# Kernel optimization log

Measured on AMD Instinct MI355X. Metric: run time of the kernel, lower is better.

## Reference

```python
import jax, jax.numpy as jnp
import numpy as np

L = 2            # decoder layers (layer slice)
H = 1024         # hidden size
NH = 16          # attention heads
HD = 64          # head dim
NKV = 4          # kv heads (GQA)
KVD = NKV * HD   # 256
I = 2816         # intermediate size
V = 32000        # vocab
R = 64           # lora rank
S = 512          # seq len
B = 1            # batch
BLK = 64         # quantization block size
NCODE = 16       # 2**k codebook entries (k=4)
LORA_S = 16.0 / 64.0  # lora_alpha / lora_r
EPS = 1e-6
THETA = 10000.0


def _dequant(idx2d, am, codebook):
    # blockwise k-bit dequant: w[i] = codebook[idx[i]] * absmax[i // BLK]
    n, k = idx2d.shape
    w = codebook[idx2d.reshape(-1)].reshape(-1, BLK) * am[:, None]
    return w.reshape(n, k)


def _linear(x, idx, am, codebook, A, Bm):
    # fused dequant-matmul + low-rank LoRA update
    w = _dequant(idx, am, codebook)           # [N, K]
    return x @ w.T + LORA_S * ((x @ A.T) @ Bm.T)


def _rmsnorm(x, w):
    return x * jax.lax.rsqrt(jnp.mean(x * x, axis=-1, keepdims=True) + EPS) * w


def _rope_cache():
    inv_freq = 1.0 / (THETA ** (np.arange(0, HD, 2, dtype=np.float32) / HD))
    freqs = np.outer(np.arange(S, dtype=np.float32), inv_freq)
    emb = np.concatenate([freqs, freqs], axis=-1)  # [S, HD]
    return jnp.asarray(np.cos(emb)), jnp.asarray(np.sin(emb))


def _apply_rope(x, cos, sin):
    # x: [B, S, n_heads, HD]; llama-style non-interleaved rotate_half
    x1, x2 = jnp.split(x, 2, axis=-1)
    rot = jnp.concatenate([-x2, x1], axis=-1)
    return x * cos[None, :, None, :] + rot * sin[None, :, None, :]


def _forward(input_ids, embed, codebook, q_idx, q_am, qA, qB, k_idx, k_am, kA, kB,
             v_idx, v_am, vA, vB, o_idx, o_am, oA, oB, g_idx, g_am, gA, gB,
             u_idx, u_am, uA, uB, d_idx, d_am, dA, dB, ln1, ln2, final_norm,
             lm_idx, lm_am):
    cos, sin = _rope_cache()
    mask = jnp.tril(jnp.ones((S, S), dtype=bool))
    h = embed[input_ids]  # [B, S, H]
    for i in range(L):
        # --- attention block ---
        x = _rmsnorm(h, ln1[i])
        q = _linear(x, q_idx[i], q_am[i], codebook, qA[i], qB[i]).reshape(B, S, NH, HD)
        k = _linear(x, k_idx[i], k_am[i], codebook, kA[i], kB[i]).reshape(B, S, NKV, HD)
        v = _linear(x, v_idx[i], v_am[i], codebook, vA[i], vB[i]).reshape(B, S, NKV, HD)
        q = _apply_rope(q, cos, sin)
        k = _apply_rope(k, cos, sin)
        k = jnp.repeat(k, NH // NKV, axis=2)  # GQA expand
        v = jnp.repeat(v, NH // NKV, axis=2)
        scores = jnp.einsum('bqhd,bkhd->bhqk', q, k) / np.float32(np.sqrt(HD))
        scores = jnp.where(mask[None, None], scores, jnp.float32(-1e30))
        attn = jax.nn.softmax(scores, axis=-1)
        ctx = jnp.einsum('bhqk,bkhd->bqhd', attn, v).reshape(B, S, H)
        h = h + _linear(ctx, o_idx[i], o_am[i], codebook, oA[i], oB[i])
        # --- SwiGLU MLP block ---
        x = _rmsnorm(h, ln2[i])
        gate = _linear(x, g_idx[i], g_am[i], codebook, gA[i], gB[i])
        up = _linear(x, u_idx[i], u_am[i], codebook, uA[i], uB[i])
        h = h + _linear(jax.nn.silu(gate) * up, d_idx[i], d_am[i], codebook, dA[i], dB[i])
    h = _rmsnorm(h, final_norm)
    logits = h @ _dequant(lm_idx, lm_am, codebook).T  # quantized lm_head, no LoRA
    return logits


def setup_inputs():
    key = jax.random.key(0)
    keys = iter(jax.random.split(key, 80))
    def idx(shape):
        return jax.random.randint(next(keys), shape, 0, NCODE, dtype=jnp.int32)
    def amL(nblocks):
        return jax.random.uniform(next(keys), (L, nblocks), dtype=jnp.float32) * 0.02 + 1e-3
    def lora(shape):
        return jax.random.normal(next(keys), shape, dtype=jnp.float32) * 0.02
    inp = {}
    inp['input_ids'] = jax.random.randint(next(keys), (B, S), 0, V, dtype=jnp.int32)
    inp['embed'] = jax.random.normal(next(keys), (V, H), dtype=jnp.float32) * 0.02
    inp['codebook'] = jnp.linspace(-1.0, 1.0, NCODE, dtype=jnp.float32)
    inp['q_idx'] = idx((L, H, H));    inp['q_am'] = amL(H * H // BLK)
    inp['qA'] = lora((L, R, H));      inp['qB'] = lora((L, H, R))
    inp['k_idx'] = idx((L, KVD, H));  inp['k_am'] = amL(KVD * H // BLK)
    inp['kA'] = lora((L, R, H));      inp['kB'] = lora((L, KVD, R))
    inp['v_idx'] = idx((L, KVD, H));  inp['v_am'] = amL(KVD * H // BLK)
    inp['vA'] = lora((L, R, H));      inp['vB'] = lora((L, KVD, R))
    inp['o_idx'] = idx((L, H, H));    inp['o_am'] = amL(H * H // BLK)
    inp['oA'] = lora((L, R, H));      inp['oB'] = lora((L, H, R))
    inp['g_idx'] = idx((L, I, H));    inp['g_am'] = amL(I * H // BLK)
    inp['gA'] = lora((L, R, H));      inp['gB'] = lora((L, I, R))
    inp['u_idx'] = idx((L, I, H));    inp['u_am'] = amL(I * H // BLK)
    inp['uA'] = lora((L, R, H));      inp['uB'] = lora((L, I, R))
    inp['d_idx'] = idx((L, H, I));    inp['d_am'] = amL(H * I // BLK)
    inp['dA'] = lora((L, R, I));      inp['dB'] = lora((L, H, R))
    inp['ln1'] = jnp.ones((L, H), dtype=jnp.float32)
    inp['ln2'] = jnp.ones((L, H), dtype=jnp.float32)
    inp['final_norm'] = jnp.ones((H,), dtype=jnp.float32)
    inp['lm_idx'] = idx((V, H))
    inp['lm_am'] = jax.random.uniform(next(keys), (V * H // BLK,), dtype=jnp.float32) * 0.02 + 1e-3
    return inp


def reference(input_ids, embed, codebook, q_idx, q_am, qA, qB, k_idx, k_am, kA, kB,
              v_idx, v_am, vA, vB, o_idx, o_am, oA, oB, g_idx, g_am, gA, gB,
              u_idx, u_am, uA, uB, d_idx, d_am, dA, dB, ln1, ln2, final_norm,
              lm_idx, lm_am):
    return _forward(input_ids, embed, codebook, q_idx, q_am, qA, qB, k_idx, k_am, kA, kB,
                    v_idx, v_am, vA, vB, o_idx, o_am, oA, oB, g_idx, g_am, gA, gB,
                    u_idx, u_am, uA, uB, d_idx, d_am, dA, dB, ln1, ln2, final_norm,
                    lm_idx, lm_am)
```

## Files before the change

kernel.cpp:

```cpp
#include <hip/hip_runtime.h>
#include <math.h>

constexpr int LAYERS = 2;
constexpr int H      = 1024;
constexpr int NH     = 16;
constexpr int HD     = 64;
constexpr int NKV    = 4;
constexpr int KVD    = 256;
constexpr int IDIM   = 2816;
constexpr int VOCAB  = 32000;
constexpr int RR     = 64;
constexpr int SEQ    = 512;
constexpr float LORA_SCALE = 0.25f;
constexpr float RMS_EPS    = 1e-6f;

typedef __attribute__((ext_vector_type(8))) __bf16 bf16x8;
typedef __attribute__((ext_vector_type(4))) __bf16 bf16x4;
typedef __attribute__((ext_vector_type(4))) float f32x4;

__device__ __forceinline__ float dot4(float4 a, float4 b) {
    return a.x*b.x + a.y*b.y + a.z*b.z + a.w*b.w;
}

__device__ __forceinline__ bf16x8 pack8(float4 a, float4 b) {
    bf16x8 p;
    p[0] = (__bf16)a.x; p[1] = (__bf16)a.y; p[2] = (__bf16)a.z; p[3] = (__bf16)a.w;
    p[4] = (__bf16)b.x; p[5] = (__bf16)b.y; p[6] = (__bf16)b.z; p[7] = (__bf16)b.w;
    return p;
}

__device__ __forceinline__ bf16x8 dq8(int4 a, int4 b, float amv, const float* cbs) {
    bf16x8 p;
    p[0] = (__bf16)(cbs[a.x]*amv); p[1] = (__bf16)(cbs[a.y]*amv);
    p[2] = (__bf16)(cbs[a.z]*amv); p[3] = (__bf16)(cbs[a.w]*amv);
    p[4] = (__bf16)(cbs[b.x]*amv); p[5] = (__bf16)(cbs[b.y]*amv);
    p[6] = (__bf16)(cbs[b.z]*amv); p[7] = (__bf16)(cbs[b.w]*amv);
    return p;
}

__global__ __launch_bounds__(256) void k_embed(const int* __restrict__ ids,
                                               const float* __restrict__ embed,
                                               float* __restrict__ h) {
    int s = blockIdx.x;
    int t = threadIdx.x;
    const float4* src = (const float4*)(embed + (size_t)ids[s] * H);
    float4* dst = (float4*)(h + (size_t)s * H);
    dst[t] = src[t];
}

__global__ __launch_bounds__(256) void k_rmsnorm(const float* __restrict__ h,
                                                 const float* __restrict__ w,
                                                 __bf16* __restrict__ x) {
    __shared__ float red[4];
    int s = blockIdx.x, t = threadIdx.x;
    float4 a = ((const float4*)(h + (size_t)s * H))[t];
    float ss = a.x*a.x + a.y*a.y + a.z*a.z + a.w*a.w;
    #pragma unroll
    for (int o = 32; o > 0; o >>= 1) ss += __shfl_xor(ss, o, 64);
    if ((t & 63) == 0) red[t >> 6] = ss;
    __syncthreads();
    float tot = red[0] + red[1] + red[2] + red[3];
    float scale = rsqrtf(tot * (1.0f / H) + RMS_EPS);
    float4 wv = ((const float4*)w)[t];
    bf16x4 o4;
    o4[0] = (__bf16)(a.x*scale*wv.x); o4[1] = (__bf16)(a.y*scale*wv.y);
    o4[2] = (__bf16)(a.z*scale*wv.z); o4[3] = (__bf16)(a.w*scale*wv.w);
    *(bf16x4*)&x[(size_t)s * H + t * 4] = o4;
}

struct GSeg {
    const int* widx; const float* am; const float* lA; const float* lB;
    float* y; int N; int ntiles;
};

template<int NSEG, bool LORA, int EPI, int KSPLIT>
__global__ __launch_bounds__(256) void k_gemm(
    const __bf16* __restrict__ x, const float* __restrict__ cb,
    GSeg s0, GSeg s1, GSeg s2, int K, int ntTotal, __bf16* __restrict__ y2)
{
    __shared__ __align__(16) __bf16 As[128][64];
    __shared__ __align__(16) __bf16 Bs[128][64];
    __shared__ __align__(16) __bf16 La[LORA ? 64 : 1][64];
    __shared__ float cbs[16];

    const int id = blockIdx.x + (blockIdx.y << 2);
    const int mtile = (id >> 3) & 3;
    int n = ((id >> 5) << 3) + (id & 7);
    if (n >= ntTotal) return;

    const int* widx; const float* am; const float* lA; const float* lB;
    float* y; int N;
    if (NSEG == 1 || n < s0.ntiles) {
        widx=s0.widx; am=s0.am; lA=s0.lA; lB=s0.lB; y=s0.y; N=s0.N;
    } else if (NSEG == 2 || (n - s0.ntiles) < s1.ntiles) {
        n -= s0.ntiles;
        widx=s1.widx; am=s1.am; lA=s1.lA; lB=s1.lB; y=s1.y; N=s1.N;
    } else {
        n -= s0.ntiles + s1.ntiles;
        widx=s2.widx; am=s2.am; lA=s2.lA; lB=s2.lB; y=s2.y; N=s2.N;
    }
    const int sbase = mtile * 128;
    const int nbase = n * 128;
    const int t    = threadIdx.x;
    const int lane = t & 63;
    const int wave = t >> 6;
    const int wm = (wave >> 1) * 64;
    const int wn = (wave & 1) * 64;
    if (t < 16) cbs[t] = cb[t];
    const int srow = t >> 3;
    const int scol = (t & 7) * 8;
    const int KB   = K >> 6;

    int kbLo, kbHi;
    if constexpr (KSPLIT > 1) {
        kbLo = ((int)blockIdx.z * KB) / KSPLIT;
        kbHi = (((int)blockIdx.z + 1) * KB) / KSPLIT;
    } else { kbLo = 0; kbHi = KB; }

    f32x4 acc[4][4];
    f32x4 accl[4][4];
    const f32x4 fz = {0.f, 0.f, 0.f, 0.f};
    #pragma unroll
    for (int i = 0; i < 4; ++i)
        #pragma unroll
        for (int j = 0; j < 4; ++j) { acc[i][j] = fz; if constexpr (LORA) accl[i][j] = fz; }

    __syncthreads();

    for (int kb = kbLo; kb < kbHi; ++kb) {
        const int k0 = kb << 6;
        #pragma unroll
        for (int p = 0; p < 4; ++p) {
            int row = p * 32 + srow;
            *(bf16x8*)&As[row][scol] =
                *(const bf16x8*)&x[(size_t)(sbase + row) * K + k0 + scol];
        }
        #pragma unroll
        for (int p = 0; p < 4; ++p) {
            int row = p * 32 + srow;
            const int* ip = &widx[(size_t)(nbase + row) * K + k0 + scol];
            int4 i0 = *(const int4*)ip;
            int4 i1 = *(const int4*)(ip + 4);
            float amv = am[(size_t)(nbase + row) * KB + kb];
            *(bf16x8*)&Bs[row][scol] = dq8(i0, i1, amv, cbs);
        }
        if constexpr (LORA) {
            #pragma unroll
            for (int p = 0; p < 2; ++p) {
                int r = p * 32 + srow;
                const float* lp = &lA[(size_t)r * K + k0 + scol];
                *(bf16x8*)&La[r][scol] = pack8(*(const float4*)lp, *(const float4*)(lp + 4));
            }
        }
        __syncthreads();
        #pragma unroll
        for (int s = 0; s < 2; ++s) {
            bf16x8 a[4], b[4];
            #pragma unroll
            for (int mi = 0; mi < 4; ++mi)
                a[mi] = *(bf16x8*)&As[wm + mi*16 + (lane & 15)][s*32 + (lane >> 4)*8];
            #pragma unroll
            for (int ni = 0; ni < 4; ++ni)
                b[ni] = *(bf16x8*)&Bs[wn + ni*16 + (lane & 15)][s*32 + (lane >> 4)*8];
            #pragma unroll
            for (int mi = 0; mi < 4; ++mi)
                #pragma unroll
                for (int ni = 0; ni < 4; ++ni)
                    acc[mi][ni] = __builtin_amdgcn_mfma_f32_16x16x32_bf16(
                        a[mi], b[ni], acc[mi][ni], 0, 0, 0);
            if constexpr (LORA) {
                bf16x8 bl[4];
                #pragma unroll
                for (int ni = 0; ni < 4; ++ni)
                    bl[ni] = *(bf16x8*)&La[ni*16 + (lane & 15)][s*32 + (lane >> 4)*8];
                #pragma unroll
                for (int mi = 0; mi < 4; ++mi)
                    #pragma unroll
                    for (int ni = 0; ni < 4; ++ni)
                        accl[mi][ni] = __builtin_amdgcn_mfma_f32_16x16x32_bf16(
                            a[mi], bl[ni], accl[mi][ni], 0, 0, 0);
            }
        }
        __syncthreads();
    }

    if constexpr (LORA) {
        if (wn == 0) {
            const int cr = (lane >> 4) * 4, cc = lane & 15;
            #pragma unroll
            for (int mi = 0; mi < 4; ++mi)
                #pragma unroll
                for (int ni = 0; ni < 4; ++ni)
                    #pragma unroll
                    for (int r = 0; r < 4; ++r)
                        As[wm + mi*16 + cr + r][ni*16 + cc] =
                            (__bf16)(LORA_SCALE * accl[mi][ni][r]);
        }
        #pragma unroll
        for (int p = 0; p < 4; ++p) {
            int row = p * 32 + srow;
            const float* bp = &lB[(size_t)(nbase + row) * RR + scol];
            *(bf16x8*)&Bs[row][scol] = pack8(*(const float4*)bp, *(const float4*)(bp + 4));
        }
        __syncthreads();
        #pragma unroll
        for (int s = 0; s < 2; ++s) {
            bf16x8 a[4], b[4];
            #pragma unroll
            for (int mi = 0; mi < 4; ++mi)
                a[mi] = *(bf16x8*)&As[wm + mi*16 + (lane & 15)][s*32 + (lane >> 4)*8];
            #pragma unroll
            for (int ni = 0; ni < 4; ++ni)
                b[ni] = *(bf16x8*)&Bs[wn + ni*16 + (lane & 15)][s*32 + (lane >> 4)*8];
            #pragma unroll
            for (int mi = 0; mi < 4; ++mi)
                #pragma unroll
                for (int ni = 0; ni < 4; ++ni)
                    acc[mi][ni] = __builtin_amdgcn_mfma_f32_16x16x32_bf16(
                        a[mi], b[ni], acc[mi][ni], 0, 0, 0);
        }
    }

    const int cr = (lane >> 4) * 4;
    const int cc = lane & 15;
    #pragma unroll
    for (int mi = 0; mi < 4; ++mi) {
        #pragma unroll
        for (int ni = 0; ni < 4; ++ni) {
            int gr = sbase + wm + mi * 16 + cr;
            int gc = nbase + wn + ni * 16 + cc;
            #pragma unroll
            for (int r = 0; r < 4; ++r) {
                size_t off = (size_t)(gr + r) * N + gc;
                if constexpr (EPI == 0) {
                    if constexpr (KSPLIT > 1) atomicAdd(&y[off], acc[mi][ni][r]);
                    else                      y[off] = acc[mi][ni][r];
                }
                if constexpr (EPI == 1) {
                    if constexpr (KSPLIT > 1) atomicAdd(&y[off], acc[mi][ni][r]);
                    else                      y[off] += acc[mi][ni][r];
                }
            }
        }
    }
    (void)y2;
}

__global__ __launch_bounds__(256) void k_silu(const float* __restrict__ g,
                                              const float* __restrict__ u,
                                              __bf16* __restrict__ out, int n4) {
    int i = blockIdx.x * 256 + threadIdx.x;
    int stride = gridDim.x * 256;
    for (; i < n4; i += stride) {
        float4 gv = ((const float4*)g)[i];
        float4 uv = ((const float4*)u)[i];
        bf16x4 o4;
        o4[0] = (__bf16)(gv.x / (1.f + __expf(-gv.x)) * uv.x);
        o4[1] = (__bf16)(gv.y / (1.f + __expf(-gv.y)) * uv.y);
        o4[2] = (__bf16)(gv.z / (1.f + __expf(-gv.z)) * uv.z);
        o4[3] = (__bf16)(gv.w / (1.f + __expf(-gv.w)) * uv.w);
        *(bf16x4*)&out[(size_t)i * 4] = o4;
    }
}

__global__ __launch_bounds__(256) void k_rope(float* __restrict__ q, float* __restrict__ k) {
    int s  = blockIdx.x;
    int hs = blockIdx.y * 4 + (threadIdx.x >> 6);
    int d  = threadIdx.x & 63;
    float* p = (hs < NH) ? q + ((size_t)s * NH + hs) * HD
                         : k + ((size_t)s * NKV + (hs - NH)) * HD;
    int j = d & 31;
    float inv = exp2f(-(float)(2 * j) * (13.287712379549449f / 64.0f));
    float ang = (float)s * inv;
    float sn, c;
    __sincosf(ang, &sn, &c);
    float xv = p[d];
    float other = (d < 32) ? -p[d + 32] : p[d - 32];
    p[d] = xv * c + other * sn;
}

__global__ __launch_bounds__(256) void k_scores(const float* __restrict__ q,
                                                const float* __restrict__ k,
                                                float* __restrict__ attn) {
    int qt = blockIdx.x;
    int h  = blockIdx.y;
    int kvh = h >> 2;
    __shared__ float qs[16][68];
    __shared__ float ks[64][68];
    __shared__ float sc[16][528];
    int t = threadIdx.x;
    { int row = t >> 4; int c4 = (t & 15) << 2;
      *(float4*)&qs[row][c4] = *(const float4*)&q[(size_t)(qt*16 + row) * H + h * HD + c4]; }
    for (int c = 0; c < 8; ++c) {
        #pragma unroll
        for (int i = 0; i < 4; ++i) {
            int id = t + i * 256; int row = id >> 4; int c4 = (id & 15) << 2;
            *(float4*)&ks[row][c4] = *(const float4*)&k[(size_t)(c*64 + row) * KVD + kvh * HD + c4];
        }
        __syncthreads();
        int r  = t >> 4;
        int cc = (t & 15) << 2;
        float4 acc = make_float4(0.f, 0.f, 0.f, 0.f);
        #pragma unroll
        for (int kk = 0; kk < 64; kk += 4) {
            float4 a = *(const float4*)&qs[r][kk];
            acc.x += dot4(a, *(const float4*)&ks[cc + 0][kk]);
            acc.y += dot4(a, *(const float4*)&ks[cc + 1][kk]);
            acc.z += dot4(a, *(const float4*)&ks[cc + 2][kk]);
            acc.w += dot4(a, *(const float4*)&ks[cc + 3][kk]);
        }
        acc.x *= 0.125f; acc.y *= 0.125f; acc.z *= 0.125f; acc.w *= 0.125f;
        *(float4*)&sc[r][c * 64 + cc] = acc;
        __syncthreads();
    }
    int r = t >> 4, lane = t & 15;
    int qpos = qt * 16 + r;
    float mx = -1e30f;
    for (int c = lane; c < SEQ; c += 16) if (c <= qpos) mx = fmaxf(mx, sc[r][c]);
    #pragma unroll
    for (int o = 8; o > 0; o >>= 1) mx = fmaxf(mx, __shfl_xor(mx, o, 16));
    float sum = 0.f;
    for (int c = lane; c < SEQ; c += 16) {
        float e = (c <= qpos) ? __expf(sc[r][c] - mx) : 0.f;
        sc[r][c] = e; sum += e;
    }
    #pragma unroll
    for (int o = 8; o > 0; o >>= 1) sum += __shfl_xor(sum, o, 16);
    float inv = 1.0f / sum;
    for (int c = lane; c < SEQ; c += 16)
        attn[((size_t)h * SEQ + qpos) * SEQ + c] = sc[r][c] * inv;
}

__global__ __launch_bounds__(256) void k_ctx(const float* __restrict__ attn,
                                             const float* __restrict__ v,
                                             __bf16* __restrict__ ctx) {
    int qt = blockIdx.x, h = blockIdx.y, kvh = h >> 2;
    __shared__ float as_[64][68];
    __shared__ float vs[64][68];
    int t = threadIdx.x;
    float acc[4][4] = {};
    for (int c = 0; c <= qt; ++c) {
        #pragma unroll
        for (int i = 0; i < 4; ++i) {
            int id = t + i * 256; int row = id >> 4; int c4 = (id & 15) << 2;
            *(float4*)&as_[row][c4] = *(const float4*)&attn[((size_t)h*SEQ + qt*64 + row) * SEQ + c*64 + c4];
            *(float4*)&vs[row][c4]  = *(const float4*)&v[(size_t)(c*64 + row) * KVD + kvh * HD + c4];
        }
        __syncthreads();
        int ty = (t >> 4) * 4, tx = (t & 15) * 4;
        #pragma unroll
        for (int kk = 0; kk < 64; ++kk) {
            float4 b = *(const float4*)&vs[kk][tx];
            #pragma unroll
            for (int i = 0; i < 4; ++i) {
                float a = as_[ty + i][kk];
                acc[i][0] += a * b.x; acc[i][1] += a * b.y;
                acc[i][2] += a * b.z; acc[i][3] += a * b.w;
            }
        }
        __syncthreads();
    }
    int ty = (t >> 4) * 4, tx = (t & 15) * 4;
    #pragma unroll
    for (int i = 0; i < 4; ++i) {
        bf16x4 o4;
        o4[0] = (__bf16)acc[i][0]; o4[1] = (__bf16)acc[i][1];
        o4[2] = (__bf16)acc[i][2]; o4[3] = (__bf16)acc[i][3];
        *(bf16x4*)&ctx[(size_t)(qt*64 + ty + i) * H + h * HD + tx] = o4;
    }
}

extern "C" void kernel_launch(void* const* d_in, const int* in_sizes, int n_in,
                              void* d_out, int out_size, void* d_ws, size_t ws_size,
                              hipStream_t stream) {
    const int*   p_ids   = (const int*)  d_in[0];
    const float* p_embed = (const float*)d_in[1];
    const float* p_cb    = (const float*)d_in[2];
    const int*   p_qidx  = (const int*)  d_in[3];  const float* p_qam = (const float*)d_in[4];
    const float* p_qA    = (const float*)d_in[5];  const float* p_qB  = (const float*)d_in[6];
    const int*   p_kidx  = (const int*)  d_in[7];  const float* p_kam = (const float*)d_in[8];
    const float* p_kA    = (const float*)d_in[9];  const float* p_kB  = (const float*)d_in[10];
    const int*   p_vidx  = (const int*)  d_in[11]; const float* p_vam = (const float*)d_in[12];
    const float* p_vA    = (const float*)d_in[13]; const float* p_vB  = (const float*)d_in[14];
    const int*   p_oidx  = (const int*)  d_in[15]; const float* p_oam = (const float*)d_in[16];
    const float* p_oA    = (const float*)d_in[17]; const float* p_oB  = (const float*)d_in[18];
    const int*   p_gidx  = (const int*)  d_in[19]; const float* p_gam = (const float*)d_in[20];
    const float* p_gA    = (const float*)d_in[21]; const float* p_gB  = (const float*)d_in[22];
    const int*   p_uidx  = (const int*)  d_in[23]; const float* p_uam = (const float*)d_in[24];
    const float* p_uA    = (const float*)d_in[25]; const float* p_uB  = (const float*)d_in[26];
    const int*   p_didx  = (const int*)  d_in[27]; const float* p_dam = (const float*)d_in[28];
    const float* p_dA    = (const float*)d_in[29]; const float* p_dB  = (const float*)d_in[30];
    const float* p_ln1   = (const float*)d_in[31];
    const float* p_ln2   = (const float*)d_in[32];
    const float* p_fn    = (const float*)d_in[33];
    const int*   p_lmidx = (const int*)  d_in[34]; const float* p_lmam = (const float*)d_in[35];

    char* w = (char*)d_ws;
    const size_t MB = 1024 * 1024;
    float*  hbuf  = (float*) (w + 0);
    __bf16* xb16  = (__bf16*)(w + 2*MB);
    float*  qb    = (float*) (w + 3*MB);
    float*  kb    = (float*) (w + 5*MB);
    float*  vb    = (float*) (w + 5*MB + 512*1024);
    __bf16* ctx16 = (__bf16*)(w + 6*MB);
    float*  attn  = (float*) (w + 7*MB);
    __bf16* g16   = (__bf16*)(w + 7*MB);
    float*  gatef = (float*) (w + 11*MB);
    float*  upf   = (float*) (w + 17*MB);

    const GSeg znull = {nullptr, nullptr, nullptr, nullptr, nullptr, 0, 0};
    const size_t mlpB = (size_t)SEQ * IDIM * sizeof(float);

    k_embed<<<SEQ, 256, 0, stream>>>(p_ids, p_embed, hbuf);

    for (int l = 0; l < LAYERS; ++l) {
        const int*   qi  = p_qidx + (size_t)l * H * H;      const float* qa = p_qam + (size_t)l * (H*H/64);
        const float* qAl = p_qA + (size_t)l * RR * H;       const float* qBl = p_qB + (size_t)l * H * RR;
        const int*   ki  = p_kidx + (size_t)l * KVD * H;    const float* ka = p_kam + (size_t)l * (KVD*H/64);
        const float* kAl = p_kA + (size_t)l * RR * H;       const float* kBl = p_kB + (size_t)l * KVD * RR;
        const int*   vi  = p_vidx + (size_t)l * KVD * H;    const float* va = p_vam + (size_t)l * (KVD*H/64);
        const float* vAl = p_vA + (size_t)l * RR * H;       const float* vBl = p_vB + (size_t)l * KVD * RR;
        const int*   oi  = p_oidx + (size_t)l * H * H;      const float* oa = p_oam + (size_t)l * (H*H/64);
        const float* oAl = p_oA + (size_t)l * RR * H;       const float* oBl = p_oB + (size_t)l * H * RR;
        const int*   gi  = p_gidx + (size_t)l * IDIM * H;   const float* ga = p_gam + (size_t)l * (IDIM*H/64);
        const float* gAl = p_gA + (size_t)l * RR * H;       const float* gBl = p_gB + (size_t)l * IDIM * RR;
        const int*   ui  = p_uidx + (size_t)l * IDIM * H;   const float* ua = p_uam + (size_t)l * (IDIM*H/64);
        const float* uAl = p_uA + (size_t)l * RR * H;       const float* uBl = p_uB + (size_t)l * IDIM * RR;
        const int*   di  = p_didx + (size_t)l * H * IDIM;   const float* da = p_dam + (size_t)l * (H*IDIM/64);
        const float* dAl = p_dA + (size_t)l * RR * IDIM;    const float* dBl = p_dB + (size_t)l * H * RR;

        k_rmsnorm<<<SEQ, 256, 0, stream>>>(hbuf, p_ln1 + (size_t)l * H, xb16);
        hipMemsetAsync(qb, 0, 3*MB, stream);
        {
            GSeg sq = {qi, qa, qAl, qBl, qb, H,   8};
            GSeg sk = {ki, ka, kAl, kBl, kb, KVD, 2};
            GSeg sv = {vi, va, vAl, vBl, vb, KVD, 2};
            k_gemm<3,true,0,8><<<dim3(4,16,8), 256, 0, stream>>>(
                xb16, p_cb, sq, sk, sv, H, 12, nullptr);
        }
        k_rope<<<dim3(SEQ, 5), 256, 0, stream>>>(qb, kb);
        k_scores<<<dim3(SEQ/16, NH), 256, 0, stream>>>(qb, kb, attn);
        k_ctx<<<dim3(SEQ/64, NH), 256, 0, stream>>>(attn, vb, ctx16);
        {
            GSeg so = {oi, oa, oAl, oBl, hbuf, H, 8};
            k_gemm<1,true,1,8><<<dim3(4,8,8), 256, 0, stream>>>(
                ctx16, p_cb, so, znull, znull, H, 8, nullptr);
        }

        k_rmsnorm<<<SEQ, 256, 0, stream>>>(hbuf, p_ln2 + (size_t)l * H, xb16);
        hipMemsetAsync(gatef, 0, mlpB, stream);
        {
            GSeg sg = {gi, ga, gAl, gBl, gatef, IDIM, 22};
            k_gemm<1,true,0,4><<<dim3(4,24,4), 256, 0, stream>>>(
                xb16, p_cb, sg, znull, znull, H, 22, nullptr);
        }
        hipMemsetAsync(upf, 0, mlpB, stream);
        {
            GSeg su = {ui, ua, uAl, uBl, upf, IDIM, 22};
            k_gemm<1,true,0,4><<<dim3(4,24,4), 256, 0, stream>>>(
                xb16, p_cb, su, znull, znull, H, 22, nullptr);
        }
        k_silu<<<1024, 256, 0, stream>>>(gatef, upf, g16, SEQ * IDIM / 4);
        {
            GSeg sd = {di, da, dAl, dBl, hbuf, H, 8};
            k_gemm<1,true,1,11><<<dim3(4,8,11), 256, 0, stream>>>(
                g16, p_cb, sd, znull, znull, IDIM, 8, nullptr);
        }
    }

    k_rmsnorm<<<SEQ, 256, 0, stream>>>(hbuf, p_fn, xb16);
    {
        GSeg sl = {p_lmidx, p_lmam, nullptr, nullptr, (float*)d_out, VOCAB, 250};
        k_gemm<1,false,0,1><<<dim3(4,256), 256, 0, stream>>>(
            xb16, p_cb, sl, znull, znull, H, 250, nullptr);
    }
}
```

Before: 997.5 us.

## Prefetch next K tile into registers, swizzle LDS tiles, replicate codebook per slot

The GEMM main loop now loads the next K-block's activations, weight indices and absmax into registers while MFMAs run on the current shared-memory tile. This hides global load latency behind compute. Shared-memory tiles use an XOR swizzle on columns to cut bank conflicts on the MFMA fragment reads, and the LoRA staging writes are swizzled to match. The 16-entry codebook is replicated across 32 bank slots so divergent index lookups do not conflict. In exchange the prefetch raises register pressure, which may lower occupancy.

```diff
diff --git a/kernel.cpp b/kernel.cpp
--- a/kernel.cpp
+++ b/kernel.cpp
@@ -29,12 +29,13 @@
     return p;
 }
 
-__device__ __forceinline__ bf16x8 dq8(int4 a, int4 b, float amv, const float* cbs) {
+__device__ __forceinline__ bf16x8 dq8(int4 a, int4 b, float amv,
+                                      const float cbt[16][32], int slot) {
     bf16x8 p;
-    p[0] = (__bf16)(cbs[a.x]*amv); p[1] = (__bf16)(cbs[a.y]*amv);
-    p[2] = (__bf16)(cbs[a.z]*amv); p[3] = (__bf16)(cbs[a.w]*amv);
-    p[4] = (__bf16)(cbs[b.x]*amv); p[5] = (__bf16)(cbs[b.y]*amv);
-    p[6] = (__bf16)(cbs[b.z]*amv); p[7] = (__bf16)(cbs[b.w]*amv);
+    p[0] = (__bf16)(cbt[a.x][slot]*amv); p[1] = (__bf16)(cbt[a.y][slot]*amv);
+    p[2] = (__bf16)(cbt[a.z][slot]*amv); p[3] = (__bf16)(cbt[a.w][slot]*amv);
+    p[4] = (__bf16)(cbt[b.x][slot]*amv); p[5] = (__bf16)(cbt[b.y][slot]*amv);
+    p[6] = (__bf16)(cbt[b.z][slot]*amv); p[7] = (__bf16)(cbt[b.w][slot]*amv);
     return p;
 }
 
@@ -81,7 +82,7 @@
     __shared__ __align__(16) __bf16 As[128][64];
     __shared__ __align__(16) __bf16 Bs[128][64];
     __shared__ __align__(16) __bf16 La[LORA ? 64 : 1][64];
-    __shared__ float cbs[16];
+    __shared__ float cbt[16][32];
 
     const int id = blockIdx.x + (blockIdx.y << 2);
     const int mtile = (id >> 3) & 3;
@@ -106,9 +107,12 @@
     const int wave = t >> 6;
     const int wm = (wave >> 1) * 64;
     const int wn = (wave & 1) * 64;
-    if (t < 16) cbs[t] = cb[t];
+    const int slot = t & 31;
+    for (int i = t; i < 512; i += 256) (&cbt[0][0])[i] = cb[i >> 5];
     const int srow = t >> 3;
     const int scol = (t & 7) * 8;
+    const int wsw  = (srow & 7) << 3;
+    const int rsw  = (lane & 7) << 3;
     const int KB   = K >> 6;
 
     int kbLo, kbHi;
@@ -125,6 +129,21 @@
         #pragma unroll
         for (int j = 0; j < 4; ++j) { acc[i][j] = fz; if constexpr (LORA) accl[i][j] = fz; }
 
+    bf16x8 pa[4]; int4 pi0[4], pi1[4]; float pam[4];
+    auto LOADT = [&](int kb_) {
+        const int k0_ = kb_ << 6;
+        #pragma unroll
+        for (int p = 0; p < 4; ++p) {
+            const int row_ = p * 32 + srow;
+            pa[p] = *(const bf16x8*)&x[(size_t)(sbase + row_) * K + k0_ + scol];
+            const int* ip_ = &widx[(size_t)(nbase + row_) * K + k0_ + scol];
+            pi0[p] = ((const int4*)ip_)[0];
+            pi1[p] = ((const int4*)ip_)[1];
+            pam[p] = am[(size_t)(nbase + row_) * KB + kb_];
+        }
+    };
+
+    LOADT(kbLo);
     __syncthreads();
 
     for (int kb = kbLo; kb < kbHi; ++kb) {
@@ -132,36 +151,28 @@
         #pragma unroll
         for (int p = 0; p < 4; ++p) {
             int row = p * 32 + srow;
-            *(bf16x8*)&As[row][scol] =
-                *(const bf16x8*)&x[(size_t)(sbase + row) * K + k0 + scol];
-        }
-        #pragma unroll
-        for (int p = 0; p < 4; ++p) {
-            int row = p * 32 + srow;
-            const int* ip = &widx[(size_t)(nbase + row) * K + k0 + scol];
-            int4 i0 = *(const int4*)ip;
-            int4 i1 = *(const int4*)(ip + 4);
-            float amv = am[(size_t)(nbase + row) * KB + kb];
-            *(bf16x8*)&Bs[row][scol] = dq8(i0, i1, amv, cbs);
+            *(bf16x8*)&As[row][scol ^ wsw] = pa[p];
+            *(bf16x8*)&Bs[row][scol ^ wsw] = dq8(pi0[p], pi1[p], pam[p], cbt, slot);
         }
         if constexpr (LORA) {
             #pragma unroll
             for (int p = 0; p < 2; ++p) {
                 int r = p * 32 + srow;
                 const float* lp = &lA[(size_t)r * K + k0 + scol];
-                *(bf16x8*)&La[r][scol] = pack8(*(const float4*)lp, *(const float4*)(lp + 4));
+                *(bf16x8*)&La[r][scol ^ wsw] = pack8(*(const float4*)lp, *(const float4*)(lp + 4));
             }
         }
         __syncthreads();
+        if (kb + 1 < kbHi) LOADT(kb + 1);
         #pragma unroll
         for (int s = 0; s < 2; ++s) {
             bf16x8 a[4], b[4];
             #pragma unroll
             for (int mi = 0; mi < 4; ++mi)
-                a[mi] = *(bf16x8*)&As[wm + mi*16 + (lane & 15)][s*32 + (lane >> 4)*8];
+                a[mi] = *(bf16x8*)&As[wm + mi*16 + (lane & 15)][(s*32 + (lane >> 4)*8) ^ rsw];
             #pragma unroll
             for (int ni = 0; ni < 4; ++ni)
-                b[ni] = *(bf16x8*)&Bs[wn + ni*16 + (lane & 15)][s*32 + (lane >> 4)*8];
+                b[ni] = *(bf16x8*)&Bs[wn + ni*16 + (lane & 15)][(s*32 + (lane >> 4)*8) ^ rsw];
             #pragma unroll
             for (int mi = 0; mi < 4; ++mi)
                 #pragma unroll
@@ -172,7 +183,7 @@
                 bf16x8 bl[4];
                 #pragma unroll
                 for (int ni = 0; ni < 4; ++ni)
-                    bl[ni] = *(bf16x8*)&La[ni*16 + (lane & 15)][s*32 + (lane >> 4)*8];
+                    bl[ni] = *(bf16x8*)&La[ni*16 + (lane & 15)][(s*32 + (lane >> 4)*8) ^ rsw];
                 #pragma unroll
                 for (int mi = 0; mi < 4; ++mi)
                     #pragma unroll
@@ -192,15 +203,17 @@
                 #pragma unroll
                 for (int ni = 0; ni < 4; ++ni)
                     #pragma unroll
-                    for (int r = 0; r < 4; ++r)
-                        As[wm + mi*16 + cr + r][ni*16 + cc] =
+                    for (int r = 0; r < 4; ++r) {
+                        int row = wm + mi*16 + cr + r;
+                        As[row][(ni*16 + cc) ^ ((row & 7) << 3)] =
                             (__bf16)(LORA_SCALE * accl[mi][ni][r]);
+                    }
         }
         #pragma unroll
         for (int p = 0; p < 4; ++p) {
             int row = p * 32 + srow;
             const float* bp = &lB[(size_t)(nbase + row) * RR + scol];
-            *(bf16x8*)&Bs[row][scol] = pack8(*(const float4*)bp, *(const float4*)(bp + 4));
+            *(bf16x8*)&Bs[row][scol ^ wsw] = pack8(*(const float4*)bp, *(const float4*)(bp + 4));
         }
         __syncthreads();
         #pragma unroll
@@ -208,10 +221,10 @@
             bf16x8 a[4], b[4];
             #pragma unroll
             for (int mi = 0; mi < 4; ++mi)
-                a[mi] = *(bf16x8*)&As[wm + mi*16 + (lane & 15)][s*32 + (lane >> 4)*8];
+                a[mi] = *(bf16x8*)&As[wm + mi*16 + (lane & 15)][(s*32 + (lane >> 4)*8) ^ rsw];
             #pragma unroll
             for (int ni = 0; ni < 4; ++ni)
-                b[ni] = *(bf16x8*)&Bs[wn + ni*16 + (lane & 15)][s*32 + (lane >> 4)*8];
+                b[ni] = *(bf16x8*)&Bs[wn + ni*16 + (lane & 15)][(s*32 + (lane >> 4)*8) ^ rsw];
             #pragma unroll
             for (int mi = 0; mi < 4; ++mi)
                 #pragma unroll
```

Result: no change. 1.003 ms (+0.6%).
